# Kernel optimization log

Hardware: AMD Instinct MI355X
Metric: run time of the kernel (lower is better)

The kernel has to match this reference:

```python
import jax, jax.numpy as jnp
import numpy as np

INPUT_DIM = 2048
NUM_EXPERTS = 64
TOP_K = 2


def setup_inputs() -> dict:
    key = jax.random.key(0)
    kx, kw, kb = jax.random.split(key, 3)
    x = jax.random.normal(kx, (4, 4096, INPUT_DIM), dtype=jnp.float32)
    # nn.Linear default init: U(-1/sqrt(fan_in), 1/sqrt(fan_in))
    bound = 1.0 / np.sqrt(INPUT_DIM)
    W = jax.random.uniform(kw, (INPUT_DIM, NUM_EXPERTS), dtype=jnp.float32, minval=-bound, maxval=bound)
    b = jax.random.uniform(kb, (NUM_EXPERTS,), dtype=jnp.float32, minval=-bound, maxval=bound)
    return {"x": x, "W": W, "b": b}


def reference(x, W, b):
    # dropout p=0.0 -> identity
    logits = jnp.einsum("bsd,de->bse", x, W) + b            # [B,S,E]
    topk_logits, topk_idx = jax.lax.top_k(logits, TOP_K)     # [B,S,K]
    topk_w = jax.nn.softmax(topk_logits, axis=-1)            # softmax over top-k only
    # scatter top-k weights back to full expert dim; non-top-k stay zero
    onehot = jax.nn.one_hot(topk_idx, NUM_EXPERTS, dtype=topk_w.dtype)  # [B,S,K,E]
    weights = jnp.einsum("bsk,bske->bse", topk_w, onehot)
    return weights
```

## Files before the change

### kernel.cpp

```cpp
#include <hip/hip_runtime.h>
#include <math.h>

#define D 2048
#define E 64
#define EH 32
#define TOK 64
#define THREADS 1024
#define NKC 8
#define KCH (D / NKC)

typedef float f16v __attribute__((ext_vector_type(16)));

__device__ __forceinline__ void wload(f16v (&dst)[2], const float* p) {
    dst[0] = *(const f16v*)(p);
    dst[1] = *(const f16v*)(p + 16);
}

__device__ __forceinline__ void fmagrp(float (&acc)[EH], float xj,
                                       const f16v (&wb)[2]) {
#pragma unroll
    for (int h = 0; h < 2; ++h)
#pragma unroll
        for (int i = 0; i < 16; ++i)
            acc[h * 16 + i] = fmaf(xj, wb[h][i], acc[h * 16 + i]);
}

__device__ __forceinline__ void tile_write(float* base, const float (&acc)[EH],
                                           int lane) {
#pragma unroll
    for (int c = 0; c < 8; ++c) {
        int s = (c + lane) & 7;
        float4 v = {acc[4 * c], acc[4 * c + 1], acc[4 * c + 2], acc[4 * c + 3]};
        *(float4*)(base + lane * EH + s * 4) = v;
    }
}

__device__ __forceinline__ void tile_add(const float* base, float (&acc)[EH],
                                         int lane) {
#pragma unroll
    for (int c = 0; c < 8; ++c) {
        int s = (c + lane) & 7;
        float4 v = *(const float4*)(base + lane * EH + s * 4);
        acc[4 * c] += v.x; acc[4 * c + 1] += v.y;
        acc[4 * c + 2] += v.z; acc[4 * c + 3] += v.w;
    }
}

__global__ __launch_bounds__(THREADS, 4)
void gating_kernel(const float* __restrict__ x,
                   const float* __restrict__ W,
                   const float* __restrict__ Bv,
                   float* __restrict__ out)
{
    __shared__ __align__(16) char smem[65536];

    const int tid  = threadIdx.x;
    const int lane = tid & 63;
    const int w    = __builtin_amdgcn_readfirstlane(tid >> 6);
    const int eh   = w & 1;
    const int kc   = w >> 1;
    const int tok0 = blockIdx.x * TOK;

    const float* xrow = x + (size_t)(tok0 + lane) * D + kc * KCH;
    const float* wk   = W + (size_t)kc * KCH * E + eh * EH;

    float acc[EH];
#pragma unroll
    for (int e = 0; e < EH; ++e) acc[e] = 0.f;

    f16v wb[2][2];
    wload(wb[0], wk);
    wload(wb[1], wk + E);
    float4 xv = *(const float4*)(xrow);
    float4 xn = *(const float4*)(xrow + 4);

#pragma unroll 1
    for (int k4 = 0; k4 < KCH / 4; ++k4) {
        float4 xc = xv; xv = xn;
        int nx = (k4 + 2 < KCH / 4) ? k4 + 2 : KCH / 4 - 1;
        xn = *(const float4*)(xrow + nx * 4);
#pragma unroll
        for (int j = 0; j < 4; ++j) {
            const float xj = j == 0 ? xc.x : j == 1 ? xc.y
                           : j == 2 ? xc.z : xc.w;
            fmagrp(acc, xj, wb[j & 1]);
            int r = 4 * k4 + j + 2;
            if (r > KCH - 1) r = KCH - 1;
            wload(wb[j & 1], wk + (size_t)r * E);
        }
    }

    float* tiles = (float*)smem;
    __syncthreads();
    if (w >= 8) tile_write(tiles + (w - 8) * 2048, acc, lane);
    __syncthreads();
    if (w < 8)  tile_add(tiles + w * 2048, acc, lane);
    __syncthreads();
    if (w >= 4 && w < 8) tile_write(tiles + (w - 4) * 2048, acc, lane);
    __syncthreads();
    if (w < 4)  tile_add(tiles + w * 2048, acc, lane);
    __syncthreads();
    if (w == 2 || w == 3) tile_write(tiles + (w - 2) * 2048, acc, lane);
    __syncthreads();
    if (w < 2)  tile_add(tiles + w * 2048, acc, lane);
    __syncthreads();

    float* logits = (float*)smem;
    float* sw1 = (float*)(smem + 16640);
    float* sw2 = (float*)(smem + 16896);
    int*   si1 = (int*)  (smem + 17152);
    int*   si2 = (int*)  (smem + 17408);

    if (w < 2) {
#pragma unroll
        for (int e = 0; e < EH; ++e)
            logits[lane * 65 + eh * EH + e] = acc[e];
    }
    __syncthreads();

    if (w == 0) {
        float m1 = -3.4e38f, m2 = -3.4e38f;
        int i1 = 0, i2 = 0;
#pragma unroll
        for (int e = 0; e < E; ++e) {
            float v = logits[lane * 65 + e] + Bv[e];
            if (v > m1)      { m2 = m1; i2 = i1; m1 = v; i1 = e; }
            else if (v > m2) { m2 = v; i2 = e; }
        }
        float p = 1.0f / (1.0f + expf(m2 - m1));
        sw1[lane] = p; sw2[lane] = 1.0f - p;
        si1[lane] = i1; si2[lane] = i2;
    }
    __syncthreads();

    float4* o4 = (float4*)(out + (size_t)tok0 * E);
    {
        int idx = tid;
        int tl  = idx >> 4;
        int e0  = (idx & 15) * 4;
        int a1 = si1[tl], a2 = si2[tl];
        float v1 = sw1[tl], v2 = sw2[tl];
        float4 v;
        v.x = (e0 + 0 == a1) ? v1 : (e0 + 0 == a2) ? v2 : 0.0f;
        v.y = (e0 + 1 == a1) ? v1 : (e0 + 1 == a2) ? v2 : 0.0f;
        v.z = (e0 + 2 == a1) ? v1 : (e0 + 2 == a2) ? v2 : 0.0f;
        v.w = (e0 + 3 == a1) ? v1 : (e0 + 3 == a2) ? v2 : 0.0f;
        o4[idx] = v;
    }
}

extern "C" void kernel_launch(void* const* d_in, const int* in_sizes, int n_in,
                              void* d_out, int out_size, void* d_ws, size_t ws_size,
                              hipStream_t stream) {
    const float* x = (const float*)d_in[0];
    const float* W = (const float*)d_in[1];
    const float* b = (const float*)d_in[2];
    float* out = (float*)d_out;

    const int tokens = in_sizes[0] / D;
    const int blocks = tokens / TOK;

    gating_kernel<<<blocks, THREADS, 0, stream>>>(x, W, b, out);
}
```

Before: 259.3 us.

## Restructure gating GEMM into register tiles with LDS double-buffered W

Replaces the lane-per-token scheme with a 32-token, 256-thread block where each lane computes an 8-token by 4-expert register tile. Four waves split the K dimension. W chunks are staged through double-buffered shared memory with register prefetch. The cross-wave reduction tree shrinks from 16 waves to 4. The aim is more reuse of each W value per load and less reduction overhead. In exchange, each lane's x reads are strided across eight rows, and the block has less parallelism.

Result: slower. 416.6 us (+60.6%).

```diff
diff --git a/kernel.cpp b/kernel.cpp
--- a/kernel.cpp
+++ b/kernel.cpp
@@ -3,122 +3,131 @@
 
 #define D 2048
 #define E 64
-#define EH 32
-#define TOK 64
-#define THREADS 1024
-#define NKC 8
-#define KCH (D / NKC)
+#define NW 4
+#define THREADS 256
+#define TOK 32
+#define KCH (D / NW)
+#define BK 8
+#define NIT (KCH / BK)
 
-typedef float f16v __attribute__((ext_vector_type(16)));
+#define SMEM_BYTES 25216
 
-__device__ __forceinline__ void wload(f16v (&dst)[2], const float* p) {
-    dst[0] = *(const f16v*)(p);
-    dst[1] = *(const f16v*)(p + 16);
+__device__ __forceinline__ void tile_write(float* base, const float4 (&acc)[8],
+                                           int tr, int ec) {
+#pragma unroll
+    for (int tt = 0; tt < 8; ++tt)
+        *(float4*)(base + (tr + 4 * tt) * 64 + ec * 4) = acc[tt];
 }
 
-__device__ __forceinline__ void fmagrp(float (&acc)[EH], float xj,
-                                       const f16v (&wb)[2]) {
+__device__ __forceinline__ void tile_add(const float* base, float4 (&acc)[8],
+                                         int tr, int ec) {
 #pragma unroll
-    for (int h = 0; h < 2; ++h)
-#pragma unroll
-        for (int i = 0; i < 16; ++i)
-            acc[h * 16 + i] = fmaf(xj, wb[h][i], acc[h * 16 + i]);
-}
-
-__device__ __forceinline__ void tile_write(float* base, const float (&acc)[EH],
-                                           int lane) {
-#pragma unroll
-    for (int c = 0; c < 8; ++c) {
-        int s = (c + lane) & 7;
-        float4 v = {acc[4 * c], acc[4 * c + 1], acc[4 * c + 2], acc[4 * c + 3]};
-        *(float4*)(base + lane * EH + s * 4) = v;
+    for (int tt = 0; tt < 8; ++tt) {
+        float4 v = *(const float4*)(base + (tr + 4 * tt) * 64 + ec * 4);
+        acc[tt].x += v.x; acc[tt].y += v.y;
+        acc[tt].z += v.z; acc[tt].w += v.w;
     }
 }
 
-__device__ __forceinline__ void tile_add(const float* base, float (&acc)[EH],
-                                         int lane) {
-#pragma unroll
-    for (int c = 0; c < 8; ++c) {
-        int s = (c + lane) & 7;
-        float4 v = *(const float4*)(base + lane * EH + s * 4);
-        acc[4 * c] += v.x; acc[4 * c + 1] += v.y;
-        acc[4 * c + 2] += v.z; acc[4 * c + 3] += v.w;
-    }
-}
-
-__global__ __launch_bounds__(THREADS, 4)
+__global__ __launch_bounds__(THREADS, 2)
 void gating_kernel(const float* __restrict__ x,
                    const float* __restrict__ W,
                    const float* __restrict__ Bv,
                    float* __restrict__ out)
 {
-    __shared__ __align__(16) char smem[65536];
+    __shared__ __align__(16) char smem[SMEM_BYTES];
 
     const int tid  = threadIdx.x;
     const int lane = tid & 63;
-    const int w    = __builtin_amdgcn_readfirstlane(tid >> 6);
-    const int eh   = w & 1;
-    const int kc   = w >> 1;
+    const int w    = tid >> 6;
     const int tok0 = blockIdx.x * TOK;
+    const int tr = lane & 3;
+    const int ec = lane >> 2;
 
-    const float* xrow = x + (size_t)(tok0 + lane) * D + kc * KCH;
-    const float* wk   = W + (size_t)kc * KCH * E + eh * EH;
+    const float* xb[8];
+#pragma unroll
+    for (int tt = 0; tt < 8; ++tt)
+        xb[tt] = x + (size_t)(tok0 + tr + 4 * tt) * D + w * KCH;
 
-    float acc[EH];
+    const float* wg = W + (size_t)w * KCH * E;
+    float* sbase = (float*)(smem + w * 4096);
+
+    float4 acc[8];
 #pragma unroll
-    for (int e = 0; e < EH; ++e) acc[e] = 0.f;
+    for (int tt = 0; tt < 8; ++tt) acc[tt] = float4{0.f, 0.f, 0.f, 0.f};
 
-    f16v wb[2][2];
-    wload(wb[0], wk);
-    wload(wb[1], wk + E);
-    float4 xv = *(const float4*)(xrow);
-    float4 xn = *(const float4*)(xrow + 4);
+    float4 wr0 = *(const float4*)(wg + lane * 4);
+    float4 wr1 = *(const float4*)(wg + 256 + lane * 4);
+    *(float4*)(sbase + lane * 4) = wr0;
+    *(float4*)(sbase + 256 + lane * 4) = wr1;
+    wr0 = *(const float4*)(wg + 512 + lane * 4);
+    wr1 = *(const float4*)(wg + 512 + 256 + lane * 4);
 
 #pragma unroll 1
-    for (int k4 = 0; k4 < KCH / 4; ++k4) {
-        float4 xc = xv; xv = xn;
-        int nx = (k4 + 2 < KCH / 4) ? k4 + 2 : KCH / 4 - 1;
-        xn = *(const float4*)(xrow + nx * 4);
+    for (int it = 0; it < NIT; ++it) {
+        if (it + 1 < NIT) {
+            float* nb = sbase + ((it + 1) & 1) * 512;
+            *(float4*)(nb + lane * 4) = wr0;
+            *(float4*)(nb + 256 + lane * 4) = wr1;
+        }
+        if (it + 2 < NIT) {
+            wr0 = *(const float4*)(wg + (it + 2) * 512 + lane * 4);
+            wr1 = *(const float4*)(wg + (it + 2) * 512 + 256 + lane * 4);
+        }
+        const float* ws = sbase + (it & 1) * 512;
+
 #pragma unroll
-        for (int j = 0; j < 4; ++j) {
-            const float xj = j == 0 ? xc.x : j == 1 ? xc.y
-                           : j == 2 ? xc.z : xc.w;
-            fmagrp(acc, xj, wb[j & 1]);
-            int r = 4 * k4 + j + 2;
-            if (r > KCH - 1) r = KCH - 1;
-            wload(wb[j & 1], wk + (size_t)r * E);
+        for (int u = 0; u < 2; ++u) {
+            float4 A[8];
+#pragma unroll
+            for (int tt = 0; tt < 8; ++tt)
+                A[tt] = *(const float4*)(xb[tt] + it * BK + u * 4);
+#pragma unroll
+            for (int j = 0; j < 4; ++j) {
+                float4 bf = *(const float4*)(ws + (u * 4 + j) * 64 + ec * 4);
+#pragma unroll
+                for (int tt = 0; tt < 8; ++tt) {
+                    const float av = j == 0 ? A[tt].x : j == 1 ? A[tt].y
+                                   : j == 2 ? A[tt].z : A[tt].w;
+                    acc[tt].x = fmaf(av, bf.x, acc[tt].x);
+                    acc[tt].y = fmaf(av, bf.y, acc[tt].y);
+                    acc[tt].z = fmaf(av, bf.z, acc[tt].z);
+                    acc[tt].w = fmaf(av, bf.w, acc[tt].w);
+                }
+            }
         }
     }
 
-    float* tiles = (float*)smem;
+    float* t0 = (float*)smem;
+    float* t1 = (float*)(smem + 8192);
     __syncthreads();
-    if (w >= 8) tile_write(tiles + (w - 8) * 2048, acc, lane);
+    if (w >= 2) tile_write(w == 2 ? t0 : t1, acc, tr, ec);
     __syncthreads();
-    if (w < 8)  tile_add(tiles + w * 2048, acc, lane);
+    if (w < 2)  tile_add(w == 0 ? t0 : t1, acc, tr, ec);
     __syncthreads();
-    if (w >= 4 && w < 8) tile_write(tiles + (w - 4) * 2048, acc, lane);
-    __syncthreads();
-    if (w < 4)  tile_add(tiles + w * 2048, acc, lane);
-    __syncthreads();
-    if (w == 2 || w == 3) tile_write(tiles + (w - 2) * 2048, acc, lane);
-    __syncthreads();
-    if (w < 2)  tile_add(tiles + w * 2048, acc, lane);
+    if (w == 1) tile_write(t1, acc, tr, ec);
     __syncthreads();
 
-    float* logits = (float*)smem;
-    float* sw1 = (float*)(smem + 16640);
-    float* sw2 = (float*)(smem + 16896);
-    int*   si1 = (int*)  (smem + 17152);
-    int*   si2 = (int*)  (smem + 17408);
+    float* logits = (float*)(smem + 16384);
+    float* sw1 = (float*)(smem + 24704);
+    float* sw2 = (float*)(smem + 24832);
+    int*   si1 = (int*)  (smem + 24960);
+    int*   si2 = (int*)  (smem + 25088);
 
-    if (w < 2) {
+    if (w == 0) {
+        tile_add(t1, acc, tr, ec);
 #pragma unroll
-        for (int e = 0; e < EH; ++e)
-            logits[lane * 65 + eh * EH + e] = acc[e];
+        for (int tt = 0; tt < 8; ++tt) {
+            int row = tr + 4 * tt;
+            logits[row * 65 + ec * 4 + 0] = acc[tt].x;
+            logits[row * 65 + ec * 4 + 1] = acc[tt].y;
+            logits[row * 65 + ec * 4 + 2] = acc[tt].z;
+            logits[row * 65 + ec * 4 + 3] = acc[tt].w;
+        }
     }
     __syncthreads();
 
-    if (w == 0) {
+    if (w == 0 && lane < TOK) {
         float m1 = -3.4e38f, m2 = -3.4e38f;
         int i1 = 0, i2 = 0;
 #pragma unroll
@@ -134,8 +143,9 @@
     __syncthreads();
 
     float4* o4 = (float4*)(out + (size_t)tok0 * E);
-    {
-        int idx = tid;
+#pragma unroll
+    for (int r = 0; r < 2; ++r) {
+        int idx = r * THREADS + tid;
         int tl  = idx >> 4;
         int e0  = (idx & 15) * 4;
         int a1 = si1[tl], a2 = si2[tl];
```
